# Kernel tuning notes

Hardware: AMD Instinct MI355X
Metric: run time of the kernel (lower is better)

The kernel has to match this reference:

```python
import jax, jax.numpy as jnp
import numpy as np

N_NODES = 100000
N_EDGES = 1000000
NODE_DIM = 64
EDGE_DIM = 32
N_LAYERS = 4
NUM_GAUSS = EDGE_DIM // 2
HIDDEN = 2 * NODE_DIM
NUM_GRAPHS = 64
VOCAB = 100


def setup_inputs() -> dict:
    key = jax.random.key(0)
    ks = jax.random.split(key, 16)
    atoms = jax.random.randint(ks[0], (N_NODES,), 0, VOCAB, dtype=jnp.int32)
    edge_index = jax.random.randint(ks[1], (2, N_EDGES), 0, N_NODES, dtype=jnp.int32)
    coordinates = jax.random.normal(ks[2], (N_NODES, 3), dtype=jnp.float32) * 2.0
    is_receptor = jax.random.randint(ks[3], (N_NODES,), 0, 2, dtype=jnp.int32)
    batch_ids = jnp.sort(jax.random.randint(ks[4], (N_NODES,), 0, NUM_GRAPHS, dtype=jnp.int32))
    cat_dim = 2 * NODE_DIM + EDGE_DIM  # 160
    node_embed_w = jax.random.normal(ks[5], (VOCAB, NODE_DIM), dtype=jnp.float32) * 0.02
    subunit_embed_w = jax.random.normal(ks[6], (2, EDGE_DIM // 2), dtype=jnp.float32) * 0.02
    W1 = jax.random.normal(ks[7], (N_LAYERS, cat_dim, HIDDEN), dtype=jnp.float32) * (cat_dim ** -0.5)
    b1 = jnp.zeros((N_LAYERS, HIDDEN), dtype=jnp.float32)
    W2 = jax.random.normal(ks[8], (N_LAYERS, HIDDEN, NODE_DIM), dtype=jnp.float32) * (HIDDEN ** -0.5)
    b2 = jnp.zeros((N_LAYERS, NODE_DIM), dtype=jnp.float32)
    fc_w = jax.random.normal(ks[9], (NODE_DIM, 1), dtype=jnp.float32) * (NODE_DIM ** -0.5)
    fc_b = jnp.zeros((1,), dtype=jnp.float32)
    return {"atoms": atoms, "edge_index": edge_index, "coordinates": coordinates,
            "is_receptor": is_receptor, "batch_ids": batch_ids,
            "node_embed_w": node_embed_w, "subunit_embed_w": subunit_embed_w,
            "W1": W1, "b1": b1, "W2": W2, "b2": b2, "fc_w": fc_w, "fc_b": fc_b}


def reference(atoms, edge_index, coordinates, is_receptor, batch_ids,
              node_embed_w, subunit_embed_w, W1, b1, W2, b2, fc_w, fc_b):
    src, dst = edge_index[0], edge_index[1]
    # node embedding
    h = node_embed_w[atoms]  # [N, D]
    # edge attributes: RBF of distance + intermolecular-kind embedding
    offset = jnp.linspace(0.0, 5.0, NUM_GAUSS, dtype=jnp.float32)
    coeff = -0.5 / float(5.0 / (NUM_GAUSS - 1)) ** 2
    dist = jnp.linalg.norm(coordinates[src] - coordinates[dst], axis=1)  # [E]
    rbf = jnp.exp(coeff * (dist[:, None] - offset[None, :]) ** 2)  # [E, G]
    kind = (is_receptor[src] != is_receptor[dst]).astype(jnp.int32)
    edge_attr = jnp.concatenate([rbf, subunit_embed_w[kind]], axis=1)  # [E, EDGE_DIM]
    # message passing layers (PyG source_to_target: h_i = h[dst], h_j = h[src], aggr at dst)
    for l in range(W1.shape[0]):
        m = jnp.concatenate([h[dst], h[src], edge_attr], axis=1)  # [E, 2D+EDGE_DIM]
        m = jax.nn.silu(m @ W1[l] + b1[l]) @ W2[l] + b2[l]  # [E, D]
        agg = jax.ops.segment_sum(m, dst, num_segments=h.shape[0])
        h = jax.nn.relu(h + agg)
    # global mean pool over graphs
    sums = jax.ops.segment_sum(h, batch_ids, num_segments=NUM_GRAPHS)
    counts = jax.ops.segment_sum(jnp.ones((h.shape[0],), h.dtype), batch_ids, num_segments=NUM_GRAPHS)
    pooled = sums / jnp.maximum(counts, 1.0)[:, None]
    out = pooled @ fc_w + fc_b  # [G, 1]
    return out.squeeze(-1)
```

## Files before the change

kernel.cpp:

```cpp
#include <hip/hip_runtime.h>
#include <hip/hip_bf16.h>
#include <math.h>

#define NODE_DIM  64
#define EDGE_DIM  32
#define NUM_GAUSS 16
#define HIDDEN    128
#define CAT_DIM   160
#define TBL_BINS  2048
#define TBL_SCALE 256.0f
#define L1ABSZ    (64 * 256)
#define L2SZ      (HIDDEN * NODE_DIM)
#define TBLSZ     (2 * TBL_BINS * 128)

#define NEG_L2E   (-1.442695040888963f)
#define NEG_LN2   (-0.6931471805599453f)

#define BKT_SH    9
#define BKT_SZ    512
#define NBKT_MAX  1024


typedef __attribute__((ext_vector_type(8))) short short8;
typedef __attribute__((ext_vector_type(4))) short short4v;
typedef __attribute__((ext_vector_type(4))) float float4v;
typedef __attribute__((ext_vector_type(2))) float floatx2;

static __device__ __forceinline__ short f2bf(float x) {
  __hip_bfloat16 h = __float2bfloat16(x);
  return *reinterpret_cast<short*>(&h);
}
static __device__ __forceinline__ float bf2f(short s) {
  return __uint_as_float(((unsigned)(unsigned short)s) << 16);
}
static __device__ __forceinline__ float bflo(unsigned u) { return __uint_as_float(u << 16); }
static __device__ __forceinline__ float bfhi(unsigned u) { return __uint_as_float(u & 0xffff0000u); }

#if defined(__has_builtin) && __has_builtin(__builtin_amdgcn_exp2f)
static __device__ __forceinline__ float hw_exp2(float x) { return __builtin_amdgcn_exp2f(x); }
#else
static __device__ __forceinline__ float hw_exp2(float x) { return exp2f(x); }
#endif

__global__ void k_init(const int* __restrict__ atoms, const float* __restrict__ embed_w,
                       short* __restrict__ hb, int n) {
  int stride = gridDim.x * blockDim.x;
  for (int i = blockIdx.x * blockDim.x + threadIdx.x; i < n; i += stride) {
    int p = i & 63;
    int col = (p & 3) * 16 + (p >> 2);
    hb[i] = f2bf(embed_w[atoms[i >> 6] * NODE_DIM + col]);
  }
}

__global__ void k_zero_f(float* __restrict__ p, int n) {
  int stride = gridDim.x * blockDim.x;
  for (int i = blockIdx.x * blockDim.x + threadIdx.x; i < n; i += stride) p[i] = 0.f;
}
__global__ void k_zero_i(int* __restrict__ p, int n) {
  int i = blockIdx.x * blockDim.x + threadIdx.x;
  if (i < n) p[i] = 0;
}

__global__ __launch_bounds__(256) void k_edge_pre(
    const int* __restrict__ src, const int* __restrict__ dst,
    const float* __restrict__ coords, const int* __restrict__ isr,
    int* __restrict__ rec, int* __restrict__ bkt_total, int E) {
  __shared__ int h[NBKT_MAX];
  for (int i = threadIdx.x; i < NBKT_MAX; i += 256) h[i] = 0;
  __syncthreads();
  int stride = gridDim.x * blockDim.x;
  for (int e = blockIdx.x * blockDim.x + threadIdx.x; e < E; e += stride) {
    int s = src[e], d = dst[e];
    float dx = coords[s*3+0] - coords[d*3+0];
    float dy = coords[s*3+1] - coords[d*3+1];
    float dz = coords[s*3+2] - coords[d*3+2];
    float dist = sqrtf(dx*dx + dy*dy + dz*dz);
    int bin = (int)(dist * TBL_SCALE);
    bin = (bin > TBL_BINS - 1) ? TBL_BINS - 1 : bin;
    int kind = (isr[s] != isr[d]) ? 1 : 0;
    rec[e] = (s << 12) | (kind << 11) | bin;
    atomicAdd(&h[d >> BKT_SH], 1);
  }
  __syncthreads();
  for (int i = threadIdx.x; i < NBKT_MAX; i += 256)
    if (h[i]) atomicAdd(&bkt_total[i], h[i]);
}

__global__ void k_scan_buckets(const int* __restrict__ tot, int* __restrict__ base,
                               int* __restrict__ cur) {
  __shared__ int s[NBKT_MAX];
  int t = threadIdx.x;
  int v = tot[t];
  s[t] = v;
  __syncthreads();
  for (int o = 1; o < NBKT_MAX; o <<= 1) {
    int u = (t >= o) ? s[t - o] : 0;
    __syncthreads();
    s[t] += u;
    __syncthreads();
  }
  int ex = s[t] - v;
  base[t] = ex;
  cur[t]  = ex;
}

__global__ __launch_bounds__(256) void k_passA(
    const int* __restrict__ dst, const int* __restrict__ rec,
    int* __restrict__ bkt_cursor,
    int* __restrict__ tmp_rec, unsigned short* __restrict__ tmp_dl, int E) {
  __shared__ int h[NBKT_MAX];
  __shared__ int c[NBKT_MAX];
  const int tid = threadIdx.x;
  const int chunk = (E + gridDim.x - 1) / gridDim.x;
  const int c0 = blockIdx.x * chunk;
  const int c1 = (c0 + chunk < E) ? c0 + chunk : E;
  for (int i = tid; i < NBKT_MAX; i += 256) h[i] = 0;
  __syncthreads();
  for (int e = c0 + tid; e < c1; e += 256)
    atomicAdd(&h[dst[e] >> BKT_SH], 1);
  __syncthreads();
  for (int i = tid; i < NBKT_MAX; i += 256)
    c[i] = h[i] ? atomicAdd(&bkt_cursor[i], h[i]) : 0;
  __syncthreads();
  for (int e = c0 + tid; e < c1; e += 256) {
    int d = dst[e];
    int p = atomicAdd(&c[d >> BKT_SH], 1);
    tmp_rec[p] = rec[e];
    tmp_dl[p]  = (unsigned short)(d & (BKT_SZ - 1));
  }
}

__global__ __launch_bounds__(256) void k_passB(
    const int* __restrict__ tmp_rec, const unsigned short* __restrict__ tmp_dl,
    const int* __restrict__ bkt_base,
    int* __restrict__ sd_p, int* __restrict__ colptr, int* __restrict__ cnts,
    int N, int E, int nbkt) {
  __shared__ int h[BKT_SZ];
  __shared__ int cur[BKT_SZ];
  __shared__ int ps[256];
  const int tid = threadIdx.x;
  const int b = blockIdx.x;
  const int rb = bkt_base[b];
  const int re = (b == nbkt - 1) ? E : bkt_base[b + 1];

  h[tid] = 0; h[tid + 256] = 0;
  __syncthreads();
  for (int r = rb + tid; r < re; r += 256)
    atomicAdd(&h[tmp_dl[r]], 1);
  __syncthreads();

  int a0 = h[2*tid], a1 = h[2*tid + 1];
  ps[tid] = a0 + a1;
  __syncthreads();
  for (int o = 1; o < 256; o <<= 1) {
    int u = (tid >= o) ? ps[tid - o] : 0;
    __syncthreads();
    ps[tid] += u;
    __syncthreads();
  }
  int e0 = tid ? ps[tid - 1] : 0;
  int g0 = rb + e0;
  int g1 = g0 + a0;
  cur[2*tid]     = g0;
  cur[2*tid + 1] = g1;
  int node0 = b * BKT_SZ + 2*tid;
  if (node0 < N)     { colptr[node0]     = g0; cnts[node0]     = a0; }
  if (node0 + 1 < N) { colptr[node0 + 1] = g1; cnts[node0 + 1] = a1; }
  if (b == 0 && tid == 0) colptr[N] = E;
  __syncthreads();

  for (int r = rb + tid; r < re; r += 256) {
    int dl = tmp_dl[r];
    int p = atomicAdd(&cur[dl], 1);
    sd_p[p] = tmp_rec[r];
  }
}

__global__ void k_tbl(const float* __restrict__ W1, const float* __restrict__ sub_w,
                      short* __restrict__ tbl, int total) {
  int i = blockIdx.x * 256 + threadIdx.x;
  if (i >= total) return;
  int col  = i & 127;
  int idx  = i >> 7;
  int bin  = idx & (TBL_BINS - 1);
  int kind = (idx >> 11) & 1;
  int l    = idx >> 12;
  float dist = ((float)bin + 0.5f) * (1.0f / TBL_SCALE);
  const float* W1c = W1 + (size_t)l * CAT_DIM * HIDDEN + 128 * HIDDEN;
  float acc = 0.f;
  #pragma unroll
  for (int g = 0; g < 16; ++g) {
    float t = dist - (float)g * (1.0f / 3.0f);
    acc += __expf(-4.5f * t * t) * W1c[g * 128 + col];
  }
  #pragma unroll
  for (int g = 0; g < 16; ++g)
    acc += sub_w[kind * 16 + g] * W1c[(16 + g) * 128 + col];
  tbl[(size_t)idx * 128 + (col & 15) * 8 + (col >> 4)] = f2bf(acc * NEG_L2E);
}

__global__ void k_pack_w1ab(const float* __restrict__ W1, short* __restrict__ Wp, int total) {
  int i = blockIdx.x * blockDim.x + threadIdx.x;
  if (i >= total) return;
  int l = i / L1ABSZ, r = i % L1ABSZ;
  int k = r / 256, n = r % 256;
  int kp = (k & 15) * 4 + (k >> 4);
  int kt = kp >> 5, quad = (kp >> 3) & 3, j = kp & 7;
  int srow = (n < 128) ? k : 64 + k;
  int scol = (n < 128) ? n : n - 128;
  Wp[l * L1ABSZ + ((kt*4 + quad) * 256 + n) * 8 + j] =
      f2bf(W1[(size_t)l * CAT_DIM * HIDDEN + srow * HIDDEN + scol] * NEG_L2E);
}
__global__ void k_pack_w2(const float* __restrict__ W, short* __restrict__ Wp, int total) {
  int i = blockIdx.x * blockDim.x + threadIdx.x;
  if (i >= total) return;
  int l = i / L2SZ, r = i % L2SZ;
  int k = r / NODE_DIM, n = r % NODE_DIM;
  int kp = (k & 15) * 8 + (k >> 4);
  int kt = kp >> 5, quad = (kp >> 3) & 3, j = kp & 7;
  Wp[l * L2SZ + ((kt*4 + quad) * NODE_DIM + n) * 8 + j] = f2bf(W[i]);
}

__global__ __launch_bounds__(256, 4) void k_node(
    short* __restrict__ hb,
    const short* __restrict__ Sb, const int* __restrict__ cnts,
    const short* __restrict__ W2p, const float* __restrict__ b2,
    const short* __restrict__ W1abp, const float* __restrict__ b1,
    short* __restrict__ pa, unsigned char* __restrict__ pb, int N)
{
  __shared__ short ht[64 * 72];

  const int tid  = threadIdx.x;
  const int lane = tid & 63;
  const int w    = tid >> 6;
  const int quad = lane >> 4;
  const int l16  = lane & 15;
  const int base = blockIdx.x * 64 + w * 16;

  if (W2p) {
    float4v acc[4];
    #pragma unroll
    for (int nt = 0; nt < 4; ++nt) acc[nt] = (float4v)0.f;
    const int arow = base + l16;
    const bool av = arow < N;
    #pragma unroll
    for (int kt = 0; kt < 4; ++kt) {
      short8 a = av ? *(const short8*)&Sb[(size_t)arow * 128 + kt*32 + quad*8]
                    : (short8)0;
      #pragma unroll
      for (int nt = 0; nt < 4; ++nt) {
        short8 b = *(const short8*)&W2p[((kt*4 + quad) * NODE_DIM + nt*16 + l16) * 8];
        acc[nt] = __builtin_amdgcn_mfma_f32_16x16x32_bf16(a, b, acc[nt], 0, 0, 0);
      }
    }
    float bb[4];
    #pragma unroll
    for (int nt = 0; nt < 4; ++nt) bb[nt] = b2[nt*16 + l16];
    #pragma unroll
    for (int r = 0; r < 4; ++r) {
      int row  = base + quad*4 + r;
      int lrow = w*16 + quad*4 + r;
      if (row < N) {
        float cf = (float)cnts[row];
        short4v hv = *(const short4v*)&hb[(size_t)row * 64 + l16*4];
        float v0 = fmaxf(bf2f(hv[0]) + acc[0][r] + cf * bb[0], 0.f);
        float v1 = fmaxf(bf2f(hv[1]) + acc[1][r] + cf * bb[1], 0.f);
        float v2 = fmaxf(bf2f(hv[2]) + acc[2][r] + cf * bb[2], 0.f);
        float v3 = fmaxf(bf2f(hv[3]) + acc[3][r] + cf * bb[3], 0.f);
        short4v hs = {f2bf(v0), f2bf(v1), f2bf(v2), f2bf(v3)};
        *(short4v*)&hb[(size_t)row * 64 + l16*4] = hs;
        *(short4v*)&ht[lrow * 72 + l16*4] = hs;
      } else {
        *(short4v*)&ht[lrow * 72 + l16*4] = (short4v)0;
      }
    }
  } else {
    int row = base + l16;
    #pragma unroll
    for (int c = 0; c < 2; ++c) {
      int colc = quad*16 + c*8;
      short8 v = (row < N) ? *(const short8*)&hb[(size_t)row * 64 + colc] : (short8)0;
      *(short8*)&ht[(w*16 + l16) * 72 + colc] = v;
    }
  }

  if (W1abp) {
    float4v acc[16];
    #pragma unroll
    for (int nt = 0; nt < 16; ++nt) acc[nt] = (float4v)0.f;
    #pragma unroll
    for (int kt = 0; kt < 2; ++kt) {
      short8 a = *(const short8*)&ht[(w*16 + l16) * 72 + kt*32 + quad*8];
      #pragma unroll
      for (int nt = 0; nt < 16; ++nt) {
        short8 b = *(const short8*)&W1abp[((kt*4 + quad) * 256 + nt*16 + l16) * 8];
        acc[nt] = __builtin_amdgcn_mfma_f32_16x16x32_bf16(a, b, acc[nt], 0, 0, 0);
      }
    }
    float b1a[8];
    #pragma unroll
    for (int nt = 0; nt < 8; ++nt) b1a[nt] = b1[nt*16 + l16] * NEG_L2E;
    #pragma unroll
    for (int r = 0; r < 4; ++r) {
      int row = base + quad*4 + r;
      if (row < N) {
        short8 va;
        #pragma unroll
        for (int nt = 0; nt < 8; ++nt) va[nt] = f2bf(acc[nt][r] + b1a[nt]);
        *(short8*)&pa[(size_t)row * 128 + l16*8] = va;
        int w0 = 0, w1 = 0;
        w0 = __builtin_amdgcn_cvt_pk_fp8_f32(acc[8][r],  acc[9][r],  w0, false);
        w0 = __builtin_amdgcn_cvt_pk_fp8_f32(acc[10][r], acc[11][r], w0, true);
        w1 = __builtin_amdgcn_cvt_pk_fp8_f32(acc[12][r], acc[13][r], w1, false);
        w1 = __builtin_amdgcn_cvt_pk_fp8_f32(acc[14][r], acc[15][r], w1, true);
        uint2 pk8; pk8.x = (unsigned)w0; pk8.y = (unsigned)w1;
        *(uint2*)&pb[(size_t)row * 128 + l16*8] = pk8;
      }
    }
  }
}

__global__ __launch_bounds__(256, 8) void k_gather(
    const short* __restrict__ pa, const unsigned char* __restrict__ pb,
    const short* __restrict__ tblL,
    const int* __restrict__ sd_p, const int* __restrict__ colptr,
    short* __restrict__ Sb, int N)
{
  int n = blockIdx.x * 4 + (threadIdx.x >> 6);
  if (n >= N) return;
  const int lane = threadIdx.x & 63;
  const int d2 = lane * 2;
  const int d4 = lane * 4;

  const int s = __builtin_amdgcn_readfirstlane(colptr[n]);
  const int e = __builtin_amdgcn_readfirstlane(colptr[n + 1]);

  unsigned up = *(const unsigned*)&pa[(size_t)n * 128 + d2];
  const float p0 = bflo(up), p1 = bfhi(up);
  float s0 = 0.f, s1 = 0.f;

  const char* pbB = (const char*)pb;
  const char* tbB = (const char*)tblL;

  if (e > s) {
    unsigned short ub0[4], ub1[4];
    unsigned ue0[4], ue1[4];

    auto load4 = [&](unsigned short (&ub)[4], unsigned (&ue)[4], int j) {
      #pragma unroll
      for (int t = 0; t < 4; ++t) {
        int jj = (j + t < e) ? j + t : s;
        int rc = __builtin_amdgcn_readfirstlane(sd_p[jj]);
        const char* pr = pbB + ((size_t)((unsigned)rc >> 12) << 7);
        const char* tr = tbB + ((size_t)(rc & 0xfff) << 8);
        ub[t] = *(const unsigned short*)(pr + d2);
        ue[t] = *(const unsigned*)(tr + d4);
      }
    };
    auto consume4 = [&](unsigned short (&ub)[4], unsigned (&ue)[4], int j) {
      #pragma unroll
      for (int t = 0; t < 4; ++t) {
        if (j + t < e) {
          floatx2 bv = __builtin_amdgcn_cvt_pk_f32_fp8((int)ub[t], false);
          float y0 = p0 + bv[0] + bflo(ue[t]);
          float y1 = p1 + bv[1] + bfhi(ue[t]);
          s0 += y0 * __builtin_amdgcn_rcpf(1.f + hw_exp2(y0));
          s1 += y1 * __builtin_amdgcn_rcpf(1.f + hw_exp2(y1));
        }
      }
    };

    load4(ub0, ue0, s);
    int j = s;
    for (; j + 4 < e; j += 8) {
      load4(ub1, ue1, j + 4);
      consume4(ub0, ue0, j);
      if (j + 8 < e) load4(ub0, ue0, j + 8);
      consume4(ub1, ue1, j + 4);
    }
    if (j < e) consume4(ub0, ue0, j);
  }

  s0 *= NEG_LN2;
  s1 *= NEG_LN2;
  unsigned pk = ((unsigned)(unsigned short)f2bf(s1) << 16) | (unsigned short)f2bf(s0);
  *(unsigned*)&Sb[(size_t)n * 128 + d2] = pk;
}

__global__ void k_pool(const short* __restrict__ hb, const int* __restrict__ batch_ids,
                       float* __restrict__ pooled, float* __restrict__ counts, int N) {
  int lane = threadIdx.x & 63;
  int base = blockIdx.x * 64;
  float acc = 0.f;
  int   cnt = 0;
  int  gcur = -1;
  for (int n = 0; n < 64; ++n) {
    int node = base + n;
    if (node >= N) break;
    int g = batch_ids[node];
    if (g != gcur) {
      if (gcur >= 0) {
        atomicAdd(&pooled[gcur * NODE_DIM + lane], acc);
        if (lane == 0) atomicAdd(&counts[gcur], (float)cnt);
      }
      gcur = g; acc = 0.f; cnt = 0;
    }
    acc += bf2f(hb[(size_t)node * NODE_DIM + lane]);
    cnt++;
  }
  if (gcur >= 0) {
    atomicAdd(&pooled[gcur * NODE_DIM + lane], acc);
    if (lane == 0) atomicAdd(&counts[gcur], (float)cnt);
  }
}

__global__ void k_final(const float* __restrict__ pooled, const float* __restrict__ counts,
                        const float* __restrict__ fc_w, const float* __restrict__ fc_b,
                        float* __restrict__ out, int G) {
  int g = blockIdx.x * blockDim.x + threadIdx.x;
  if (g < G) {
    float acc = 0.f;
    for (int d = 0; d < NODE_DIM; ++d) {
      int col = (d & 3) * 16 + (d >> 2);
      acc += pooled[g * NODE_DIM + d] * fc_w[col];
    }
    float c = counts[g];
    if (c < 1.f) c = 1.f;
    out[g] = acc / c + fc_b[0];
  }
}

extern "C" void kernel_launch(void* const* d_in, const int* in_sizes, int n_in,
                              void* d_out, int out_size, void* d_ws, size_t ws_size,
                              hipStream_t stream) {
  const int*   atoms   = (const int*)  d_in[0];
  const int*   eidx    = (const int*)  d_in[1];
  const float* coords  = (const float*)d_in[2];
  const int*   isr     = (const int*)  d_in[3];
  const int*   batch   = (const int*)  d_in[4];
  const float* embed_w = (const float*)d_in[5];
  const float* sub_w   = (const float*)d_in[6];
  const float* W1      = (const float*)d_in[7];
  const float* b1      = (const float*)d_in[8];
  const float* W2      = (const float*)d_in[9];
  const float* b2      = (const float*)d_in[10];
  const float* fc_w    = (const float*)d_in[11];
  const float* fc_b    = (const float*)d_in[12];
  float* out = (float*)d_out;

  const int N = in_sizes[0];
  const int E = in_sizes[1] / 2;
  const int L = in_sizes[8] / HIDDEN;
  const int G = out_size;

  const int* srcv = eidx;
  const int* dstv = eidx + E;

  size_t off = 0;
  auto carve = [&](size_t bytes) -> char* {
    char* p = (char*)d_ws + off;
    off += (bytes + 255) & ~(size_t)255;
    return p;
  };
  short* hb       = (short*)carve((size_t)N * NODE_DIM * 2);
  short* Sb       = (short*)carve((size_t)N * HIDDEN * 2);
  short* pa       = (short*)carve((size_t)N * HIDDEN * 2);
  unsigned char* pb = (unsigned char*)carve((size_t)N * HIDDEN);
  int*   rec      = (int*)  carve((size_t)E * 4);
  int*   sd_p     = (int*)  carve((size_t)E * 4);
  int*   tmp_rec  = (int*)  carve((size_t)E * 4);
  unsigned short* tmp_dl = (unsigned short*)carve((size_t)E * 2);
  int*   cnts     = (int*)  carve((size_t)N * 4);
  int*   colptr   = (int*)  carve(((size_t)N + 2) * 4);
  int*   bkt_total  = (int*)carve((size_t)NBKT_MAX * 4);
  int*   bkt_base   = (int*)carve((size_t)(NBKT_MAX + 1) * 4);
  int*   bkt_cursor = (int*)carve((size_t)NBKT_MAX * 4);
  short* W1abp    = (short*)carve((size_t)L * L1ABSZ * 2);
  short* W2p      = (short*)carve((size_t)L * L2SZ * 2);
  short* tbl      = (short*)carve((size_t)L * TBLSZ * 2);
  float* pooled   = (float*)carve((size_t)G * NODE_DIM * 4);
  float* cntg     = (float*)carve((size_t)G * 4);

  const int nbkt = (N + BKT_SZ - 1) / BKT_SZ;

  k_zero_i<<<(NBKT_MAX + 255) / 256, 256, 0, stream>>>(bkt_total, NBKT_MAX);
  k_init<<<1024, 256, 0, stream>>>(atoms, embed_w, hb, N * NODE_DIM);
  k_edge_pre<<<512, 256, 0, stream>>>(srcv, dstv, coords, isr, rec, bkt_total, E);
  k_zero_f<<<(G * NODE_DIM + G + 255) / 256, 256, 0, stream>>>(pooled, G * NODE_DIM + G);
  k_scan_buckets<<<1, NBKT_MAX, 0, stream>>>(bkt_total, bkt_base, bkt_cursor);
  k_passA<<<256, 256, 0, stream>>>(dstv, rec, bkt_cursor, tmp_rec, tmp_dl, E);
  k_passB<<<nbkt, 256, 0, stream>>>(tmp_rec, tmp_dl, bkt_base, sd_p, colptr, cnts, N, E, nbkt);
  k_pack_w1ab<<<(L * L1ABSZ + 255) / 256, 256, 0, stream>>>(W1, W1abp, L * L1ABSZ);
  k_pack_w2<<<(L * L2SZ + 255) / 256, 256, 0, stream>>>(W2, W2p, L * L2SZ);
  k_tbl<<<(L * 2 * TBL_BINS * 128 + 255) / 256, 256, 0, stream>>>(W1, sub_w, tbl,
                                                                  L * 2 * TBL_BINS * 128);

  const int nblk_n = (N + 63) / 64;
  const int nblk_g = (N + 3) / 4;
  for (int l = 0; l < L; ++l) {
    k_node<<<nblk_n, 256, 0, stream>>>(
        hb, Sb, cnts,
        (l > 0) ? W2p + (size_t)(l - 1) * L2SZ : (const short*)nullptr,
        (l > 0) ? b2 + (size_t)(l - 1) * NODE_DIM : (const float*)nullptr,
        W1abp + (size_t)l * L1ABSZ, b1 + (size_t)l * HIDDEN,
        pa, pb, N);
    k_gather<<<nblk_g, 256, 0, stream>>>(pa, pb, tbl + (size_t)l * TBLSZ,
                                         sd_p, colptr, Sb, N);
  }
  k_node<<<nblk_n, 256, 0, stream>>>(
      hb, Sb, cnts,
      W2p + (size_t)(L - 1) * L2SZ, b2 + (size_t)(L - 1) * NODE_DIM,
      (const short*)nullptr, (const float*)nullptr, pa, pb, N);

  k_pool<<<(N + 63) / 64, 64, 0, stream>>>(hb, batch, pooled, cntg, N);
  k_final<<<1, 64, 0, stream>>>(pooled, cntg, fc_w, fc_b, out, G);
}
```

Baseline: 516.3 us.

## Fuse embedding init and mean pooling into node kernel, store pa in fp8

```diff
diff --git a/kernel.cpp b/kernel.cpp
--- a/kernel.cpp
+++ b/kernel.cpp
@@ -41,16 +41,6 @@
 #else
 static __device__ __forceinline__ float hw_exp2(float x) { return exp2f(x); }
 #endif
-
-__global__ void k_init(const int* __restrict__ atoms, const float* __restrict__ embed_w,
-                       short* __restrict__ hb, int n) {
-  int stride = gridDim.x * blockDim.x;
-  for (int i = blockIdx.x * blockDim.x + threadIdx.x; i < n; i += stride) {
-    int p = i & 63;
-    int col = (p & 3) * 16 + (p >> 2);
-    hb[i] = f2bf(embed_w[atoms[i >> 6] * NODE_DIM + col]);
-  }
-}
 
 __global__ void k_zero_f(float* __restrict__ p, int n) {
   int stride = gridDim.x * blockDim.x;
@@ -224,9 +214,12 @@
 __global__ __launch_bounds__(256, 4) void k_node(
     short* __restrict__ hb,
     const short* __restrict__ Sb, const int* __restrict__ cnts,
+    const int* __restrict__ atoms, const float* __restrict__ embed_w,
     const short* __restrict__ W2p, const float* __restrict__ b2,
     const short* __restrict__ W1abp, const float* __restrict__ b1,
-    short* __restrict__ pa, unsigned char* __restrict__ pb, int N)
+    unsigned char* __restrict__ pa, unsigned char* __restrict__ pb,
+    const int* __restrict__ batch_ids, float* __restrict__ pooled,
+    float* __restrict__ cntg, int N)
 {
   __shared__ short ht[64 * 72];
 
@@ -268,7 +261,7 @@
         float v2 = fmaxf(bf2f(hv[2]) + acc[2][r] + cf * bb[2], 0.f);
         float v3 = fmaxf(bf2f(hv[3]) + acc[3][r] + cf * bb[3], 0.f);
         short4v hs = {f2bf(v0), f2bf(v1), f2bf(v2), f2bf(v3)};
-        *(short4v*)&hb[(size_t)row * 64 + l16*4] = hs;
+        if (!pooled) *(short4v*)&hb[(size_t)row * 64 + l16*4] = hs;
         *(short4v*)&ht[lrow * 72 + l16*4] = hs;
       } else {
         *(short4v*)&ht[lrow * 72 + l16*4] = (short4v)0;
@@ -276,11 +269,20 @@
     }
   } else {
     int row = base + l16;
+    const bool rv = row < N;
+    int aid = rv ? atoms[row] : 0;
     #pragma unroll
     for (int c = 0; c < 2; ++c) {
       int colc = quad*16 + c*8;
-      short8 v = (row < N) ? *(const short8*)&hb[(size_t)row * 64 + colc] : (short8)0;
+      short8 v;
+      #pragma unroll
+      for (int k = 0; k < 8; ++k) {
+        int p = colc + k;
+        int col = (p & 3) * 16 + (p >> 2);
+        v[k] = rv ? f2bf(embed_w[aid * NODE_DIM + col]) : (short)0;
+      }
       *(short8*)&ht[(w*16 + l16) * 72 + colc] = v;
+      if (rv) *(short8*)&hb[(size_t)row * 64 + colc] = v;
     }
   }
 
@@ -304,10 +306,13 @@
     for (int r = 0; r < 4; ++r) {
       int row = base + quad*4 + r;
       if (row < N) {
-        short8 va;
-        #pragma unroll
-        for (int nt = 0; nt < 8; ++nt) va[nt] = f2bf(acc[nt][r] + b1a[nt]);
-        *(short8*)&pa[(size_t)row * 128 + l16*8] = va;
+        int a0 = 0, a1 = 0;
+        a0 = __builtin_amdgcn_cvt_pk_fp8_f32(acc[0][r] + b1a[0], acc[1][r] + b1a[1], a0, false);
+        a0 = __builtin_amdgcn_cvt_pk_fp8_f32(acc[2][r] + b1a[2], acc[3][r] + b1a[3], a0, true);
+        a1 = __builtin_amdgcn_cvt_pk_fp8_f32(acc[4][r] + b1a[4], acc[5][r] + b1a[5], a1, false);
+        a1 = __builtin_amdgcn_cvt_pk_fp8_f32(acc[6][r] + b1a[6], acc[7][r] + b1a[7], a1, true);
+        uint2 pka; pka.x = (unsigned)a0; pka.y = (unsigned)a1;
+        *(uint2*)&pa[(size_t)row * 128 + l16*8] = pka;
         int w0 = 0, w1 = 0;
         w0 = __builtin_amdgcn_cvt_pk_fp8_f32(acc[8][r],  acc[9][r],  w0, false);
         w0 = __builtin_amdgcn_cvt_pk_fp8_f32(acc[10][r], acc[11][r], w0, true);
@@ -318,10 +323,34 @@
       }
     }
   }
+
+  if (pooled) {
+    float acc = 0.f;
+    int   cnt = 0;
+    int  gcur = -1;
+    for (int i = 0; i < 16; ++i) {
+      int node = base + i;
+      if (node >= N) break;
+      int g = batch_ids[node];
+      if (g != gcur) {
+        if (gcur >= 0) {
+          atomicAdd(&pooled[gcur * NODE_DIM + lane], acc);
+          if (lane == 0) atomicAdd(&cntg[gcur], (float)cnt);
+        }
+        gcur = g; acc = 0.f; cnt = 0;
+      }
+      acc += bf2f(ht[(w*16 + i) * 72 + lane]);
+      cnt++;
+    }
+    if (gcur >= 0) {
+      atomicAdd(&pooled[gcur * NODE_DIM + lane], acc);
+      if (lane == 0) atomicAdd(&cntg[gcur], (float)cnt);
+    }
+  }
 }
 
 __global__ __launch_bounds__(256, 8) void k_gather(
-    const short* __restrict__ pa, const unsigned char* __restrict__ pb,
+    const unsigned char* __restrict__ pa, const unsigned char* __restrict__ pb,
     const short* __restrict__ tblL,
     const int* __restrict__ sd_p, const int* __restrict__ colptr,
     short* __restrict__ Sb, int N)
@@ -335,8 +364,9 @@
   const int s = __builtin_amdgcn_readfirstlane(colptr[n]);
   const int e = __builtin_amdgcn_readfirstlane(colptr[n + 1]);
 
-  unsigned up = *(const unsigned*)&pa[(size_t)n * 128 + d2];
-  const float p0 = bflo(up), p1 = bfhi(up);
+  unsigned short upa = *(const unsigned short*)&pa[(size_t)n * 128 + d2];
+  floatx2 pv = __builtin_amdgcn_cvt_pk_f32_fp8((int)upa, false);
+  const float p0 = pv[0], p1 = pv[1];
   float s0 = 0.f, s1 = 0.f;
 
   const char* pbB = (const char*)pb;
@@ -385,33 +415,6 @@
   s1 *= NEG_LN2;
   unsigned pk = ((unsigned)(unsigned short)f2bf(s1) << 16) | (unsigned short)f2bf(s0);
   *(unsigned*)&Sb[(size_t)n * 128 + d2] = pk;
-}
-
-__global__ void k_pool(const short* __restrict__ hb, const int* __restrict__ batch_ids,
-                       float* __restrict__ pooled, float* __restrict__ counts, int N) {
-  int lane = threadIdx.x & 63;
-  int base = blockIdx.x * 64;
-  float acc = 0.f;
-  int   cnt = 0;
-  int  gcur = -1;
-  for (int n = 0; n < 64; ++n) {
-    int node = base + n;
-    if (node >= N) break;
-    int g = batch_ids[node];
-    if (g != gcur) {
-      if (gcur >= 0) {
-        atomicAdd(&pooled[gcur * NODE_DIM + lane], acc);
-        if (lane == 0) atomicAdd(&counts[gcur], (float)cnt);
-      }
-      gcur = g; acc = 0.f; cnt = 0;
-    }
-    acc += bf2f(hb[(size_t)node * NODE_DIM + lane]);
-    cnt++;
-  }
-  if (gcur >= 0) {
-    atomicAdd(&pooled[gcur * NODE_DIM + lane], acc);
-    if (lane == 0) atomicAdd(&counts[gcur], (float)cnt);
-  }
 }
 
 __global__ void k_final(const float* __restrict__ pooled, const float* __restrict__ counts,
@@ -464,7 +467,7 @@
   };
   short* hb       = (short*)carve((size_t)N * NODE_DIM * 2);
   short* Sb       = (short*)carve((size_t)N * HIDDEN * 2);
-  short* pa       = (short*)carve((size_t)N * HIDDEN * 2);
+  unsigned char* pa = (unsigned char*)carve((size_t)N * HIDDEN);
   unsigned char* pb = (unsigned char*)carve((size_t)N * HIDDEN);
   int*   rec      = (int*)  carve((size_t)E * 4);
   int*   sd_p     = (int*)  carve((size_t)E * 4);
@@ -484,7 +487,6 @@
   const int nbkt = (N + BKT_SZ - 1) / BKT_SZ;
 
   k_zero_i<<<(NBKT_MAX + 255) / 256, 256, 0, stream>>>(bkt_total, NBKT_MAX);
-  k_init<<<1024, 256, 0, stream>>>(atoms, embed_w, hb, N * NODE_DIM);
   k_edge_pre<<<512, 256, 0, stream>>>(srcv, dstv, coords, isr, rec, bkt_total, E);
   k_zero_f<<<(G * NODE_DIM + G + 255) / 256, 256, 0, stream>>>(pooled, G * NODE_DIM + G);
   k_scan_buckets<<<1, NBKT_MAX, 0, stream>>>(bkt_total, bkt_base, bkt_cursor);
@@ -497,21 +499,29 @@
 
   const int nblk_n = (N + 63) / 64;
   const int nblk_g = (N + 3) / 4;
+
+  k_node<<<nblk_n, 256, 0, stream>>>(
+      hb, (const short*)nullptr, (const int*)nullptr,
+      atoms, embed_w,
+      (const short*)nullptr, (const float*)nullptr,
+      W1abp, b1, pa, pb,
+      (const int*)nullptr, (float*)nullptr, (float*)nullptr, N);
+
   for (int l = 0; l < L; ++l) {
+    const bool last = (l == L - 1);
+    k_gather<<<nblk_g, 256, 0, stream>>>(pa, pb, tbl + (size_t)l * TBLSZ,
+                                         sd_p, colptr, Sb, N);
     k_node<<<nblk_n, 256, 0, stream>>>(
         hb, Sb, cnts,
-        (l > 0) ? W2p + (size_t)(l - 1) * L2SZ : (const short*)nullptr,
-        (l > 0) ? b2 + (size_t)(l - 1) * NODE_DIM : (const float*)nullptr,
-        W1abp + (size_t)l * L1ABSZ, b1 + (size_t)l * HIDDEN,
-        pa, pb, N);
-    k_gather<<<nblk_g, 256, 0, stream>>>(pa, pb, tbl + (size_t)l * TBLSZ,
-                                         sd_p, colptr, Sb, N);
-  }
-  k_node<<<nblk_n, 256, 0, stream>>>(
-      hb, Sb, cnts,
-      W2p + (size_t)(L - 1) * L2SZ, b2 + (size_t)(L - 1) * NODE_DIM,
-      (const short*)nullptr, (const float*)nullptr, pa, pb, N);
-
-  k_pool<<<(N + 63) / 64, 64, 0, stream>>>(hb, batch, pooled, cntg, N);
+        (const int*)nullptr, (const float*)nullptr,
+        W2p + (size_t)l * L2SZ, b2 + (size_t)l * NODE_DIM,
+        last ? (const short*)nullptr : W1abp + (size_t)(l + 1) * L1ABSZ,
+        last ? (const float*)nullptr : b1 + (size_t)(l + 1) * HIDDEN,
+        pa, pb,
+        last ? batch : (const int*)nullptr,
+        last ? pooled : (float*)nullptr,
+        last ? cntg : (float*)nullptr, N);
+  }
+
   k_final<<<1, 64, 0, stream>>>(pooled, cntg, fc_w, fc_b, out, G);
 }
```

After: 542.7 us. 5.1% more time.
